# Optimization experiments

Measured on AMD Instinct MI355X. Metric: run time of the kernel, lower is better.

## Reference

```python
import jax, jax.numpy as jnp
import numpy as np

EPS = 1e-8  # torch.cosine_similarity eps


def setup_inputs() -> dict:
    key = jax.random.key(0)
    kq, km, ki = jax.random.split(key, 3)
    B, N, D = 512, 131072, 512
    query = jax.random.normal(kq, (B, D), dtype=jnp.float32)
    memory_matrix = jax.random.normal(km, (N, D), dtype=jnp.float32)
    importance = jax.random.uniform(ki, (N,), dtype=jnp.float32)
    return {"query": query, "memory_matrix": memory_matrix, "importance": importance, "k": 16}


def reference(query, memory_matrix, importance, k):
    # Cosine similarity (torch semantics: dot / max(|q||m|, eps))
    q_norm = jnp.linalg.norm(query, axis=-1)            # [B]
    m_norm = jnp.linalg.norm(memory_matrix, axis=-1)    # [N]
    dots = jnp.einsum('bd,nd->bn', query, memory_matrix)  # [B, N]
    sims = dots / jnp.maximum(q_norm[:, None] * m_norm[None, :], EPS)
    # Importance boosting
    boosted = sims * (1.0 + 0.3 * importance)[None, :]
    # Top-k retrieval + gather of memory contents
    vals, idx = jax.lax.top_k(boosted, k)               # [B, k]
    gathered = memory_matrix[idx]                        # [B, k, D]
    return vals, gathered
```

## Files before the change

kernel.cpp:

```cpp
#include <hip/hip_runtime.h>
#include <hip/hip_bf16.h>
#include <math.h>

#define BQ 512
#define DIM 512
#define NMEM 131072
#define TOPK 16

#define BM 128
#define BN 128
#define BK 32
#define KSTEPS (DIM / BK)
#define NSUB 8
#define CHUNK_N (BN * NSUB)
#define CHUNKS (NMEM / CHUNK_N)
#define BTILES (BQ / BM)
#define CAP 32
#define CAPF 24
#define RESCORE 32
#define LDSTR 40
#define NEG_INF (-3.402823466e38f)

typedef unsigned short u16;
typedef unsigned int u32;
typedef short bf16x8 __attribute__((ext_vector_type(8)));
typedef float f32x4 __attribute__((ext_vector_type(4)));

static __device__ inline u32 pack2(float a, float b) {
  __hip_bfloat162 p = __float22bfloat162_rn(make_float2(a, b));
  return *(u32*)&p;
}

static __device__ inline void gl_lds16(const void* g, void* l) {
  __builtin_amdgcn_global_load_lds(
      (const __attribute__((address_space(1))) u32*)g,
      (__attribute__((address_space(3))) u32*)l, 16, 0, 0);
}

__global__ __launch_bounds__(256) void prep_kernel(const float* __restrict__ q,
                                                   float* __restrict__ inv_qn,
                                                   u16* __restrict__ qb) {
  int row = blockIdx.x * 4 + (threadIdx.x >> 6);
  int lane = threadIdx.x & 63;
  const float4* r4 = (const float4*)(q + (size_t)row * DIM);
  float4 x0 = r4[lane * 2], x1 = r4[lane * 2 + 1];
  float ss = x0.x * x0.x + x0.y * x0.y + x0.z * x0.z + x0.w * x0.w +
             x1.x * x1.x + x1.y * x1.y + x1.z * x1.z + x1.w * x1.w;
#pragma unroll
  for (int off = 32; off; off >>= 1) ss += __shfl_down(ss, off);
  if (lane == 0) inv_qn[row] = 1.0f / sqrtf(ss);
  uint4 w;
  w.x = pack2(x0.x, x0.y);
  w.y = pack2(x0.z, x0.w);
  w.z = pack2(x1.x, x1.y);
  w.w = pack2(x1.z, x1.w);
  *(uint4*)(qb + (size_t)row * DIM + lane * 8) = w;
}

__global__ __launch_bounds__(256) void convert_kernel(
    const float* __restrict__ mem, const float* __restrict__ imp,
    u16* __restrict__ membf, float* __restrict__ colscale) {
  int row = blockIdx.x * 4 + (threadIdx.x >> 6);
  int lane = threadIdx.x & 63;
  const float4* r4 = (const float4*)(mem + (size_t)row * DIM);
  float4 x0 = r4[lane * 2], x1 = r4[lane * 2 + 1];
  float ss = x0.x * x0.x + x0.y * x0.y + x0.z * x0.z + x0.w * x0.w +
             x1.x * x1.x + x1.y * x1.y + x1.z * x1.z + x1.w * x1.w;
  uint4 w;
  w.x = pack2(x0.x, x0.y);
  w.y = pack2(x0.z, x0.w);
  w.z = pack2(x1.x, x1.y);
  w.w = pack2(x1.z, x1.w);
  *(uint4*)(membf + (size_t)row * DIM + lane * 8) = w;
#pragma unroll
  for (int off = 32; off; off >>= 1) ss += __shfl_down(ss, off);
  if (lane == 0) colscale[row] = (1.0f + 0.3f * imp[row]) / sqrtf(ss);
}

static __device__ inline void mfma_step(const u16* Asb, const u16* Bsb, int wm,
                                        int wn, int lane, f32x4 acc[4][4]) {
  bf16x8 af[4], bfr[4];
#pragma unroll
  for (int mi = 0; mi < 4; ++mi)
    af[mi] = *(const bf16x8*)&Asb[((wm << 2) + mi) * 512 + (lane << 3)];
#pragma unroll
  for (int ni = 0; ni < 4; ++ni)
    bfr[ni] = *(const bf16x8*)&Bsb[((wn << 2) + ni) * 512 + (lane << 3)];
#pragma unroll
  for (int mi = 0; mi < 4; ++mi)
#pragma unroll
    for (int ni = 0; ni < 4; ++ni)
      acc[mi][ni] = __builtin_amdgcn_mfma_f32_16x16x32_bf16(af[mi], bfr[ni],
                                                            acc[mi][ni], 0, 0, 0);
}

__global__ __launch_bounds__(256, 2) void main_fast(
    const u16* __restrict__ qb, const u16* __restrict__ membf,
    const float* __restrict__ cs, const float* __restrict__ inv_qn,
    float* __restrict__ part_v, int* __restrict__ part_i) {
  __shared__ __align__(16) u16 As[2][BM * BK];
  __shared__ __align__(16) u16 Bs[2][BN * BK];
  __shared__ float topv[BM][TOPK];
  __shared__ int topi[BM][TOPK];
  __shared__ float cbv[BM * CAPF];
  __shared__ int cbi[BM * CAPF];
  __shared__ float cutoff[BM];
  __shared__ int cnt[BM];
  __shared__ float qn_s[BM];
  __shared__ int again;

  const int tid = threadIdx.x;
  const int lane = tid & 63, wid = tid >> 6;
  const int wm = wid >> 1, wn = wid & 1;
  const int c16 = lane & 15, quad = lane >> 4;

  const int lin = blockIdx.x;
  const int btile = (lin >> 3) & 3;
  const int chunk = (lin & 7) + ((lin >> 5) << 3);
  const int bbase = btile * BM;

  const int blk0 = wid * 2;
  const u16* agA0 = qb + (size_t)(bbase + blk0 * 16 + (lane & 15)) * DIM +
                    (lane >> 4) * 8;
  const u16* bgB0 = membf +
                    (size_t)(chunk * CHUNK_N + blk0 * 16 + (lane & 15)) * DIM +
                    (lane >> 4) * 8;

  auto STAGE = [&](int gs) {
    const int p = gs & 1;
    const size_t ao = (size_t)(gs & 15) * BK;
    const size_t bo = (size_t)(gs >> 4) * (BN * DIM) + ao;
    u16* Ad = &As[p][0] + blk0 * 512;
    u16* Bd = &Bs[p][0] + blk0 * 512;
    gl_lds16(agA0 + ao, Ad);
    gl_lds16(agA0 + ao + (size_t)16 * DIM, Ad + 512);
    gl_lds16(bgB0 + bo, Bd);
    gl_lds16(bgB0 + bo + (size_t)16 * DIM, Bd + 512);
  };

  STAGE(0);
  STAGE(1);

  for (int e = tid; e < BM * TOPK; e += 256) {
    topv[e >> 4][e & 15] = NEG_INF;
    topi[e >> 4][e & 15] = -1;
  }
  if (tid < BM) {
    cutoff[tid] = NEG_INF;
    cnt[tid] = 0;
    qn_s[tid] = inv_qn[bbase + tid];
  }
  if (tid == 0) again = 0;
  __syncthreads();

  float qnl[16];
#pragma unroll
  for (int ii = 0; ii < 16; ++ii)
    qnl[ii] = qn_s[wm * 64 + (ii >> 2) * 16 + quad * 4 + (ii & 3)];

  for (int sub = 0; sub < NSUB; ++sub) {
    const int n0g = chunk * CHUNK_N + sub * BN;

    f32x4 acc[4][4];
#pragma unroll
    for (int mi = 0; mi < 4; ++mi)
#pragma unroll
      for (int ni = 0; ni < 4; ++ni) acc[mi][ni] = (f32x4){0.f, 0.f, 0.f, 0.f};

    for (int th = 0; th < KSTEPS / 2; ++th) {
      const int gs0 = sub * KSTEPS + th * 2;
      const int gs1 = gs0 + 1;
      asm volatile("s_waitcnt vmcnt(4)" ::: "memory");
      __builtin_amdgcn_s_barrier();
      mfma_step(&As[0][0], &Bs[0][0], wm, wn, lane, acc);
      __builtin_amdgcn_s_barrier();
      if (gs0 + 2 <= NSUB * KSTEPS - 1) STAGE(gs0 + 2);
      if (gs1 == NSUB * KSTEPS - 1)
        asm volatile("s_waitcnt vmcnt(0)" ::: "memory");
      else
        asm volatile("s_waitcnt vmcnt(4)" ::: "memory");
      __builtin_amdgcn_s_barrier();
      mfma_step(&As[1][0], &Bs[1][0], wm, wn, lane, acc);
      __builtin_amdgcn_s_barrier();
      if (gs1 + 2 <= NSUB * KSTEPS - 1) STAGE(gs1 + 2);
    }

    float scl[4];
    int gcol[4];
#pragma unroll
    for (int ni = 0; ni < 4; ++ni) {
      const int c = n0g + wn * 64 + ni * 16 + c16;
      scl[ni] = cs[c];
      gcol[ni] = c;
    }
#pragma unroll
    for (int mi = 0; mi < 4; ++mi)
#pragma unroll
      for (int ni = 0; ni < 4; ++ni)
#pragma unroll
        for (int reg = 0; reg < 4; ++reg)
          acc[mi][ni][reg] *= qnl[mi * 4 + reg] * scl[ni];

    unsigned long long consumed = 0ull;
    for (;;) {
      float cutl[16];
#pragma unroll
      for (int ii = 0; ii < 16; ++ii)
        cutl[ii] = cutoff[wm * 64 + (ii >> 2) * 16 + quad * 4 + (ii & 3)];
#pragma unroll
      for (int mi = 0; mi < 4; ++mi)
#pragma unroll
        for (int reg = 0; reg < 4; ++reg) {
          const int r = wm * 64 + mi * 16 + quad * 4 + reg;
          const float cl = cutl[mi * 4 + reg];
#pragma unroll
          for (int ni = 0; ni < 4; ++ni) {
            const int bit = mi * 16 + ni * 4 + reg;
            const float v = acc[mi][ni][reg];
            if (!((consumed >> bit) & 1ull) && v > cl) {
              int pos = atomicAdd(&cnt[r], 1);
              if (pos < CAPF) {
                cbv[r * CAPF + pos] = v;
                cbi[r * CAPF + pos] = gcol[ni];
                consumed |= 1ull << bit;
              }
            }
          }
        }
      __syncthreads();
      if (tid < BM) {
        const int r = tid;
        const int m = cnt[r];
        const int take = m < CAPF ? m : CAPF;
        for (int c = 0; c < take; ++c) {
          const float v = cbv[r * CAPF + c];
          const int id = cbi[r * CAPF + c];
          if (v > topv[r][TOPK - 1]) {
            int j = TOPK - 1;
            while (j > 0 && topv[r][j - 1] < v) {
              topv[r][j] = topv[r][j - 1];
              topi[r][j] = topi[r][j - 1];
              --j;
            }
            topv[r][j] = v;
            topi[r][j] = id;
          }
        }
        cutoff[r] = topv[r][TOPK - 1];
        if (m > CAPF) again = 1;
        cnt[r] = 0;
      }
      __syncthreads();
      const int more = again;
      __syncthreads();
      if (tid == 0) again = 0;
      if (!more) break;
    }
  }

  for (int e = tid; e < BM * TOPK; e += 256) {
    const int r = e >> 4, j = e & 15;
    const size_t o = ((size_t)(bbase + r) * CHUNKS + chunk) * TOPK + j;
    part_v[o] = topv[r][j];
    part_i[o] = topi[r][j];
  }
}

__global__ __launch_bounds__(256, 2) void main_kernel(
    const u16* __restrict__ qb, const float* __restrict__ mem,
    const float* __restrict__ imp, const float* __restrict__ inv_qn,
    float* __restrict__ part_v, int* __restrict__ part_i) {
  __shared__ __align__(16) u16 As[BM * LDSTR];
  __shared__ __align__(16) u16 Bs[BN * LDSTR];
  __shared__ float topv[BM][TOPK];
  __shared__ int topi[BM][TOPK];
  __shared__ float cbv[BM * CAP];
  __shared__ int cbi[BM * CAP];
  __shared__ float cutoff[BM];
  __shared__ int cnt[BM];
  __shared__ float qn_s[BM];
  __shared__ float msum[BM * 4];
  __shared__ float colscale[BN];
  __shared__ int again;

  const int tid = threadIdx.x;
  const int lane = tid & 63, wid = tid >> 6;
  const int wm = wid >> 1, wn = wid & 1;
  const int c16 = lane & 15, quad = lane >> 4;

  const int lin = blockIdx.x;
  const int btile = (lin >> 3) & 3;
  const int chunk = (lin & 7) + ((lin >> 5) << 3);
  const int bbase = btile * BM;

  for (int e = tid; e < BM * TOPK; e += 256) {
    topv[e >> 4][e & 15] = NEG_INF;
    topi[e >> 4][e & 15] = -1;
  }
  if (tid < BM) {
    cutoff[tid] = NEG_INF;
    cnt[tid] = 0;
    qn_s[tid] = inv_qn[bbase + tid];
  }
  if (tid == 0) again = 0;
  __syncthreads();

  float qnl[16];
#pragma unroll
  for (int ii = 0; ii < 16; ++ii)
    qnl[ii] = qn_s[wm * 64 + (ii >> 2) * 16 + quad * 4 + (ii & 3)];

  const int arow = tid >> 2, akc = tid & 3;
  const u16* qsrc0 = qb + (size_t)(bbase + arow) * DIM + akc * 8;
  const u16* qsrc1 = qsrc0 + (size_t)64 * DIM;
  u16* adst0 = As + arow * LDSTR + akc * 8;
  u16* adst1 = adst0 + 64 * LDSTR;
  u16* bdst0 = Bs + arow * LDSTR + akc * 8;
  u16* bdst1 = bdst0 + 64 * LDSTR;

  for (int sub = 0; sub < NSUB; ++sub) {
    const int n0g = chunk * CHUNK_N + sub * BN;
    const float* bsrc0 = mem + (size_t)(n0g + arow) * DIM + akc * 8;
    const float* bsrc1 = bsrc0 + (size_t)64 * DIM;

    f32x4 acc[4][4];
#pragma unroll
    for (int mi = 0; mi < 4; ++mi)
#pragma unroll
      for (int ni = 0; ni < 4; ++ni) acc[mi][ni] = (f32x4){0.f, 0.f, 0.f, 0.f};
    float ss0 = 0.f, ss1 = 0.f;

    for (int kt = 0; kt < DIM / BK; ++kt) {
      const int k0 = kt * BK;
      uint4 qa0 = *(const uint4*)(qsrc0 + k0);
      uint4 qa1 = *(const uint4*)(qsrc1 + k0);
      float4 b0a = *(const float4*)(bsrc0 + k0);
      float4 b0b = *(const float4*)(bsrc0 + k0 + 4);
      float4 b1a = *(const float4*)(bsrc1 + k0);
      float4 b1b = *(const float4*)(bsrc1 + k0 + 4);
      ss0 += b0a.x * b0a.x + b0a.y * b0a.y + b0a.z * b0a.z + b0a.w * b0a.w +
             b0b.x * b0b.x + b0b.y * b0b.y + b0b.z * b0b.z + b0b.w * b0b.w;
      ss1 += b1a.x * b1a.x + b1a.y * b1a.y + b1a.z * b1a.z + b1a.w * b1a.w +
             b1b.x * b1b.x + b1b.y * b1b.y + b1b.z * b1b.z + b1b.w * b1b.w;
      __syncthreads();
      *(uint4*)adst0 = qa0;
      *(uint4*)adst1 = qa1;
      uint4 w0, w1;
      w0.x = pack2(b0a.x, b0a.y); w0.y = pack2(b0a.z, b0a.w);
      w0.z = pack2(b0b.x, b0b.y); w0.w = pack2(b0b.z, b0b.w);
      w1.x = pack2(b1a.x, b1a.y); w1.y = pack2(b1a.z, b1a.w);
      w1.z = pack2(b1b.x, b1b.y); w1.w = pack2(b1b.z, b1b.w);
      *(uint4*)bdst0 = w0;
      *(uint4*)bdst1 = w1;
      __syncthreads();
      bf16x8 af[4], bfr[4];
#pragma unroll
      for (int mi = 0; mi < 4; ++mi)
        af[mi] = *(const bf16x8*)&As[(wm * 64 + mi * 16 + c16) * LDSTR + quad * 8];
#pragma unroll
      for (int ni = 0; ni < 4; ++ni)
        bfr[ni] = *(const bf16x8*)&Bs[(wn * 64 + ni * 16 + c16) * LDSTR + quad * 8];
#pragma unroll
      for (int mi = 0; mi < 4; ++mi)
#pragma unroll
        for (int ni = 0; ni < 4; ++ni)
          acc[mi][ni] = __builtin_amdgcn_mfma_f32_16x16x32_bf16(
              af[mi], bfr[ni], acc[mi][ni], 0, 0, 0);
    }

    msum[arow * 4 + akc] = ss0;
    msum[(arow + 64) * 4 + akc] = ss1;
    __syncthreads();
    if (tid < BN)
      colscale[tid] = (1.0f + 0.3f * imp[n0g + tid]) /
                      sqrtf(msum[tid * 4] + msum[tid * 4 + 1] +
                            msum[tid * 4 + 2] + msum[tid * 4 + 3]);
    __syncthreads();

    float scl[4];
    int gcol[4];
#pragma unroll
    for (int ni = 0; ni < 4; ++ni) {
      scl[ni] = colscale[wn * 64 + ni * 16 + c16];
      gcol[ni] = n0g + wn * 64 + ni * 16 + c16;
    }
#pragma unroll
    for (int mi = 0; mi < 4; ++mi)
#pragma unroll
      for (int ni = 0; ni < 4; ++ni)
#pragma unroll
        for (int reg = 0; reg < 4; ++reg)
          acc[mi][ni][reg] *= qnl[mi * 4 + reg] * scl[ni];

    unsigned long long consumed = 0ull;
    for (;;) {
      float cutl[16];
#pragma unroll
      for (int ii = 0; ii < 16; ++ii)
        cutl[ii] = cutoff[wm * 64 + (ii >> 2) * 16 + quad * 4 + (ii & 3)];
#pragma unroll
      for (int mi = 0; mi < 4; ++mi)
#pragma unroll
        for (int reg = 0; reg < 4; ++reg) {
          const int r = wm * 64 + mi * 16 + quad * 4 + reg;
          const float cl = cutl[mi * 4 + reg];
#pragma unroll
          for (int ni = 0; ni < 4; ++ni) {
            const int bit = mi * 16 + ni * 4 + reg;
            const float v = acc[mi][ni][reg];
            if (!((consumed >> bit) & 1ull) && v > cl) {
              int pos = atomicAdd(&cnt[r], 1);
              if (pos < CAP) {
                cbv[r * CAP + pos] = v;
                cbi[r * CAP + pos] = gcol[ni];
                consumed |= 1ull << bit;
              }
            }
          }
        }
      __syncthreads();
      if (tid < BM) {
        const int r = tid;
        const int m = cnt[r];
        const int take = m < CAP ? m : CAP;
        for (int c = 0; c < take; ++c) {
          const float v = cbv[r * CAP + c];
          const int id = cbi[r * CAP + c];
          if (v > topv[r][TOPK - 1]) {
            int j = TOPK - 1;
            while (j > 0 && topv[r][j - 1] < v) {
              topv[r][j] = topv[r][j - 1];
              topi[r][j] = topi[r][j - 1];
              --j;
            }
            topv[r][j] = v;
            topi[r][j] = id;
          }
        }
        cutoff[r] = topv[r][TOPK - 1];
        if (m > CAP) again = 1;
        cnt[r] = 0;
      }
      __syncthreads();
      const int more = again;
      __syncthreads();
      if (tid == 0) again = 0;
      if (!more) break;
    }
  }

  for (int e = tid; e < BM * TOPK; e += 256) {
    const int r = e >> 4, j = e & 15;
    const size_t o = ((size_t)(bbase + r) * CHUNKS + chunk) * TOPK + j;
    part_v[o] = topv[r][j];
    part_i[o] = topi[r][j];
  }
}

#define CAND (CHUNKS * TOPK)
__global__ __launch_bounds__(256) void final_kernel(
    const float* __restrict__ part_v, const int* __restrict__ part_i,
    const float* __restrict__ mem, const float* __restrict__ query,
    const float* __restrict__ imp, const float* __restrict__ inv_qn,
    float* __restrict__ out) {
  __shared__ float cv[CAND];
  __shared__ int ci[CAND];
  __shared__ float q_s[DIM];
  __shared__ float rv[4];
  __shared__ int rp[4];
  __shared__ float exv[RESCORE];
  __shared__ int exi[RESCORE];
  __shared__ float selv[TOPK];
  __shared__ int seli[TOPK];
  const int b = blockIdx.x, tid = threadIdx.x;
  const int lane = tid & 63, wid = tid >> 6;
  const size_t base = (size_t)b * CAND;
  for (int e = tid; e < CAND; e += 256) {
    cv[e] = part_v[base + e];
    ci[e] = part_i[base + e];
  }
  q_s[tid] = query[(size_t)b * DIM + tid];
  q_s[tid + 256] = query[(size_t)b * DIM + 256 + tid];
  __syncthreads();

  for (int j = 0; j < RESCORE; ++j) {
    float best = NEG_INF;
    int bp = 0;
    for (int e = tid; e < CAND; e += 256)
      if (cv[e] > best) { best = cv[e]; bp = e; }
#pragma unroll
    for (int off = 32; off; off >>= 1) {
      float ov = __shfl_down(best, off);
      int op = __shfl_down(bp, off);
      if (ov > best) { best = ov; bp = op; }
    }
    if (lane == 0) { rv[wid] = best; rp[wid] = bp; }
    __syncthreads();
    if (tid == 0) {
      float bb = rv[0];
      int pp = rp[0];
      for (int w = 1; w < 4; ++w)
        if (rv[w] > bb) { bb = rv[w]; pp = rp[w]; }
      exi[j] = ci[pp];
      cv[pp] = NEG_INF;
    }
    __syncthreads();
  }

  const float iq = inv_qn[b];
  for (int jj = wid; jj < RESCORE; jj += 4) {
    const int idx = exi[jj];
    const float4* mr = (const float4*)(mem + (size_t)idx * DIM);
    float4 m0 = mr[lane * 2], m1 = mr[lane * 2 + 1];
    float4 q0 = *(const float4*)&q_s[lane * 8];
    float4 q1 = *(const float4*)&q_s[lane * 8 + 4];
    float dt = m0.x * q0.x + m0.y * q0.y + m0.z * q0.z + m0.w * q0.w +
               m1.x * q1.x + m1.y * q1.y + m1.z * q1.z + m1.w * q1.w;
    float mm = m0.x * m0.x + m0.y * m0.y + m0.z * m0.z + m0.w * m0.w +
               m1.x * m1.x + m1.y * m1.y + m1.z * m1.z + m1.w * m1.w;
#pragma unroll
    for (int off = 32; off; off >>= 1) {
      dt += __shfl_down(dt, off);
      mm += __shfl_down(mm, off);
    }
    if (lane == 0)
      exv[jj] = dt * iq * (1.0f + 0.3f * imp[idx]) / sqrtf(mm);
  }
  __syncthreads();

  if (tid == 0) {
    u32 used = 0;
    for (int j = 0; j < TOPK; ++j) {
      float bb = NEG_INF;
      int pp = -1;
      for (int c = 0; c < RESCORE; ++c) {
        if ((used >> c) & 1u) continue;
        const float v = exv[c];
        if (v > bb || (pp >= 0 && v == bb && exi[c] < exi[pp])) { bb = v; pp = c; }
      }
      used |= 1u << pp;
      selv[j] = bb;
      seli[j] = exi[pp];
    }
  }
  __syncthreads();
  if (tid < TOPK) out[(size_t)b * TOPK + tid] = selv[tid];
  for (int e = tid; e < TOPK * (DIM / 4); e += 256) {
    const int j = e >> 7, t = e & 127;
    const float4* src = (const float4*)(mem + (size_t)seli[j] * DIM);
    float4* dst = (float4*)(out + (size_t)BQ * TOPK + ((size_t)b * TOPK + j) * DIM);
    dst[t] = src[t];
  }
}

extern "C" void kernel_launch(void* const* d_in, const int* in_sizes, int n_in,
                              void* d_out, int out_size, void* d_ws, size_t ws_size,
                              hipStream_t stream) {
  const float* query = (const float*)d_in[0];
  const float* mem = (const float*)d_in[1];
  const float* imp = (const float*)d_in[2];
  float* out = (float*)d_out;

  char* ws = (char*)d_ws;
  float* inv_qn = (float*)ws;
  u16* qb = (u16*)(ws + 2048);
  float* part_v = (float*)(ws + 2048 + (size_t)BQ * DIM * 2);
  int* part_i = (int*)((char*)part_v + (size_t)BQ * CHUNKS * TOPK * 4);
  char* extra = (char*)part_i + (size_t)BQ * CHUNKS * TOPK * 4;
  const size_t used = (size_t)(extra - ws);
  const size_t fast_need =
      used + (size_t)NMEM * 4 + (size_t)NMEM * DIM * 2;

  hipLaunchKernelGGL(prep_kernel, dim3(BQ / 4), dim3(256), 0, stream,
                     query, inv_qn, qb);
  if (ws_size >= fast_need) {
    float* colscale = (float*)extra;
    u16* membf = (u16*)(extra + (size_t)NMEM * 4);
    hipLaunchKernelGGL(convert_kernel, dim3(NMEM / 4), dim3(256), 0, stream,
                       mem, imp, membf, colscale);
    hipLaunchKernelGGL(main_fast, dim3(BTILES * CHUNKS), dim3(256), 0, stream,
                       qb, membf, colscale, inv_qn, part_v, part_i);
  } else {
    hipLaunchKernelGGL(main_kernel, dim3(BTILES * CHUNKS), dim3(256), 0, stream,
                       qb, mem, imp, inv_qn, part_v, part_i);
  }
  hipLaunchKernelGGL(final_kernel, dim3(BQ), dim3(256), 0, stream,
                     part_v, part_i, mem, query, imp, inv_qn, out);
}
```

Measured before the change: 853.1 us.

## Use unsorted min-replacement top-k with padded LDS strides and first-pass bound

Replaces the sorted insertion top-k buffer with an unsorted buffer that overwrites its current minimum slot. The minimum value and position are kept in registers. The top-k and candidate LDS arrays get odd row strides to avoid bank conflicts when each thread walks its own row. On the first filter pass of each sub-tile, it also admits values at or above a per-row bound, taken as the minimum across lanes of each lane's max. This is meant to fill the top-k quickly and raise the cutoff early, but it can push extra candidates through the single-thread merge in later sub-tiles. The per-chunk partial results are no longer sorted, which matters only if the final merge assumes sorted input.

```diff
diff --git a/kernel.cpp b/kernel.cpp
--- a/kernel.cpp
+++ b/kernel.cpp
@@ -17,6 +17,8 @@
 #define BTILES (BQ / BM)
 #define CAP 32
 #define CAPF 24
+#define TSTR 17
+#define CSTR 25
 #define RESCORE 32
 #define LDSTR 40
 #define NEG_INF (-3.402823466e38f)
@@ -100,10 +102,10 @@
     float* __restrict__ part_v, int* __restrict__ part_i) {
   __shared__ __align__(16) u16 As[2][BM * BK];
   __shared__ __align__(16) u16 Bs[2][BN * BK];
-  __shared__ float topv[BM][TOPK];
-  __shared__ int topi[BM][TOPK];
-  __shared__ float cbv[BM * CAPF];
-  __shared__ int cbi[BM * CAPF];
+  __shared__ float topv[BM * TSTR];
+  __shared__ int topi[BM * TSTR];
+  __shared__ float cbv[BM * CSTR];
+  __shared__ int cbi[BM * CSTR];
   __shared__ float cutoff[BM];
   __shared__ int cnt[BM];
   __shared__ float qn_s[BM];
@@ -142,8 +144,8 @@
   STAGE(1);
 
   for (int e = tid; e < BM * TOPK; e += 256) {
-    topv[e >> 4][e & 15] = NEG_INF;
-    topi[e >> 4][e & 15] = -1;
+    topv[(e >> 4) * TSTR + (e & 15)] = NEG_INF;
+    topi[(e >> 4) * TSTR + (e & 15)] = -1;
   }
   if (tid < BM) {
     cutoff[tid] = NEG_INF;
@@ -157,6 +159,9 @@
 #pragma unroll
   for (int ii = 0; ii < 16; ++ii)
     qnl[ii] = qn_s[wm * 64 + (ii >> 2) * 16 + quad * 4 + (ii & 3)];
+
+  float mnv = NEG_INF;
+  int mnp = 0;
 
   for (int sub = 0; sub < NSUB; ++sub) {
     const int n0g = chunk * CHUNK_N + sub * BN;
@@ -201,7 +206,20 @@
         for (int reg = 0; reg < 4; ++reg)
           acc[mi][ni][reg] *= qnl[mi * 4 + reg] * scl[ni];
 
+    float bnd[16];
+#pragma unroll
+    for (int mi = 0; mi < 4; ++mi)
+#pragma unroll
+      for (int reg = 0; reg < 4; ++reg) {
+        float mx = fmaxf(fmaxf(acc[mi][0][reg], acc[mi][1][reg]),
+                         fmaxf(acc[mi][2][reg], acc[mi][3][reg]));
+#pragma unroll
+        for (int off = 1; off < 16; off <<= 1) mx = fminf(mx, __shfl_xor(mx, off));
+        bnd[mi * 4 + reg] = mx;
+      }
+
     unsigned long long consumed = 0ull;
+    int pass0 = 1;
     for (;;) {
       float cutl[16];
 #pragma unroll
@@ -213,15 +231,18 @@
         for (int reg = 0; reg < 4; ++reg) {
           const int r = wm * 64 + mi * 16 + quad * 4 + reg;
           const float cl = cutl[mi * 4 + reg];
+          const float b = bnd[mi * 4 + reg];
 #pragma unroll
           for (int ni = 0; ni < 4; ++ni) {
             const int bit = mi * 16 + ni * 4 + reg;
             const float v = acc[mi][ni][reg];
-            if (!((consumed >> bit) & 1ull) && v > cl) {
+            const bool ok = !((consumed >> bit) & 1ull) &&
+                            (v > cl || (pass0 && v >= b));
+            if (ok) {
               int pos = atomicAdd(&cnt[r], 1);
               if (pos < CAPF) {
-                cbv[r * CAPF + pos] = v;
-                cbi[r * CAPF + pos] = gcol[ni];
+                cbv[r * CSTR + pos] = v;
+                cbi[r * CSTR + pos] = gcol[ni];
                 consumed |= 1ull << bit;
               }
             }
@@ -233,20 +254,22 @@
         const int m = cnt[r];
         const int take = m < CAPF ? m : CAPF;
         for (int c = 0; c < take; ++c) {
-          const float v = cbv[r * CAPF + c];
-          const int id = cbi[r * CAPF + c];
-          if (v > topv[r][TOPK - 1]) {
-            int j = TOPK - 1;
-            while (j > 0 && topv[r][j - 1] < v) {
-              topv[r][j] = topv[r][j - 1];
-              topi[r][j] = topi[r][j - 1];
-              --j;
+          const float v = cbv[r * CSTR + c];
+          if (v > mnv) {
+            topv[r * TSTR + mnp] = v;
+            topi[r * TSTR + mnp] = cbi[r * CSTR + c];
+            float nm = topv[r * TSTR];
+            int np = 0;
+#pragma unroll
+            for (int j = 1; j < TOPK; ++j) {
+              const float t = topv[r * TSTR + j];
+              if (t < nm) { nm = t; np = j; }
             }
-            topv[r][j] = v;
-            topi[r][j] = id;
+            mnv = nm;
+            mnp = np;
           }
         }
-        cutoff[r] = topv[r][TOPK - 1];
+        cutoff[r] = mnv;
         if (m > CAPF) again = 1;
         cnt[r] = 0;
       }
@@ -254,6 +277,7 @@
       const int more = again;
       __syncthreads();
       if (tid == 0) again = 0;
+      pass0 = 0;
       if (!more) break;
     }
   }
@@ -261,8 +285,8 @@
   for (int e = tid; e < BM * TOPK; e += 256) {
     const int r = e >> 4, j = e & 15;
     const size_t o = ((size_t)(bbase + r) * CHUNKS + chunk) * TOPK + j;
-    part_v[o] = topv[r][j];
-    part_i[o] = topi[r][j];
+    part_v[o] = topv[r * TSTR + j];
+    part_i[o] = topi[r * TSTR + j];
   }
 }
 
```

New measurement: 860.5 us. Within noise of the previous version (+0.9%).
